# Performance work log

Measured on AMD Instinct MI355X. Metric: run time of the kernel, lower is better.

## Reference

```python
import jax, jax.numpy as jnp
import numpy as np

VOCAB = 32000
D_MODEL = 1024
PATCH_LEN = 16
NHEAD = 8
B = 8
S = 4096


def setup_inputs() -> dict:
    key = jax.random.key(0)
    ks = jax.random.split(key, 8)
    token_inputs = jax.random.randint(ks[0], (B, S), 0, VOCAB, dtype=jnp.int64 if jax.config.jax_enable_x64 else jnp.int32)
    attention_mask = jax.random.randint(ks[1], (B, S), 0, 2).astype(bool)
    emb_weight = jax.random.normal(ks[2], (VOCAB, D_MODEL), dtype=jnp.float32) * 0.02
    patch_query = jax.random.normal(ks[3], (1, 1, D_MODEL), dtype=jnp.float32) * 0.02
    # nn.MultiheadAttention packed in-projection [3D, D] and out projection [D, D]
    lim = 1.0 / np.sqrt(D_MODEL)
    in_proj_w = jax.random.uniform(ks[4], (3 * D_MODEL, D_MODEL), jnp.float32, -lim, lim)
    in_proj_b = jnp.zeros((3 * D_MODEL,), jnp.float32)
    out_w = jax.random.uniform(ks[5], (D_MODEL, D_MODEL), jnp.float32, -lim, lim)
    out_b = jnp.zeros((D_MODEL,), jnp.float32)
    return {
        "token_inputs": token_inputs,
        "attention_mask": attention_mask,
        "emb_weight": emb_weight,
        "patch_query": patch_query,
        "in_proj_w": in_proj_w,
        "in_proj_b": in_proj_b,
        "out_w": out_w,
        "out_b": out_b,
    }


def reference(token_inputs, attention_mask, emb_weight, patch_query, in_proj_w, in_proj_b, out_w, out_b):
    d_model = emb_weight.shape[1]
    h, dh = NHEAD, d_model // NHEAD
    L = PATCH_LEN

    tok_emb = emb_weight[token_inputs]              # [B, S, D]
    bsz, seqlen, _ = tok_emb.shape
    # seqlen chosen divisible by PATCH_LEN -> pad_len == 0 (matches torch path)
    num_patches = seqlen // L
    BP = bsz * num_patches
    patch_tokens = tok_emb.reshape(BP, L, d_model)  # [BP, L, D]
    patch_mask = attention_mask.reshape(BP, L)      # True = valid token

    patch_valid = patch_mask.any(axis=1)            # [BP]
    # force position 0 valid for fully-empty patches (safe softmax)
    safe_mask = patch_mask | ((~patch_valid)[:, None] & (jnp.arange(L) == 0)[None, :])

    wq, wk, wv = jnp.split(in_proj_w, 3, axis=0)    # each [D, D]
    bq, bk, bv = jnp.split(in_proj_b, 3, axis=0)

    q = patch_query[0, 0] @ wq.T + bq               # [D] (same query for all patches)
    k = patch_tokens @ wk.T + bk                    # [BP, L, D]
    v = patch_tokens @ wv.T + bv                    # [BP, L, D]

    qh = q.reshape(h, dh)                           # [H, dh]
    kh = k.reshape(BP, L, h, dh)                    # [BP, L, H, dh]
    vh = v.reshape(BP, L, h, dh)

    scale = 1.0 / jnp.sqrt(jnp.asarray(dh, q.dtype))
    scores = jnp.einsum('hd,blhd->bhl', qh, kh) * scale   # [BP, H, L]
    scores = jnp.where(safe_mask[:, None, :], scores, -jnp.inf)
    attn = jax.nn.softmax(scores, axis=-1)                # [BP, H, L]

    ctx = jnp.einsum('bhl,blhd->bhd', attn, vh).reshape(BP, d_model)
    patch_latent = ctx @ out_w.T + out_b                  # [BP, D]

    patch_latent = patch_latent.reshape(bsz, num_patches, d_model)
    pv = patch_valid.reshape(bsz, num_patches)
    patch_latent = patch_latent * pv[..., None].astype(patch_latent.dtype)
    return patch_latent, pv
```

## Files before the change

kernel.cpp:

```cpp
#include <hip/hip_runtime.h>
#include <stdint.h>

#define OUT_LATENT (2048*1024)
#define SCALE 0.08838834764831845f

typedef float f32x4v __attribute__((ext_vector_type(4)));
typedef short s16x8  __attribute__((ext_vector_type(8)));

static __device__ inline unsigned short f2bf(float f) {
    union { float f; uint32_t u; } v; v.f = f;
    uint32_t u = v.u;
    return (unsigned short)((u + 0x7FFFu + ((u >> 16) & 1u)) >> 16);
}
static __device__ inline float bflo(uint32_t u) {
    union { uint32_t u; float f; } v; v.u = u << 16; return v.f;
}
static __device__ inline float bfhi(uint32_t u) {
    union { uint32_t u; float f; } v; v.u = u & 0xFFFF0000u; return v.f;
}

static __device__ __forceinline__ void async16(const unsigned short* g, unsigned short* l) {
    __builtin_amdgcn_global_load_lds(
        (const __attribute__((address_space(1))) void*)g,
        (__attribute__((address_space(3))) void*)l, 16, 0, 0);
}

__global__ __launch_bounds__(256) void k_convw(
    const float* __restrict__ wv_src, const float* __restrict__ ow_src,
    unsigned short* __restrict__ wv_dst, unsigned short* __restrict__ ow_dst) {
    int t = threadIdx.x, b = blockIdx.x;
    const float* src; unsigned short* dst; int idx;
    if (b < 1024) { src = wv_src; dst = wv_dst; idx = b * 1024 + t * 4; }
    else          { src = ow_src; dst = ow_dst; idx = (b - 1024) * 1024 + t * 4; }
    float4 f = *(const float4*)(src + idx);
    ushort4 o; o.x = f2bf(f.x); o.y = f2bf(f.y); o.z = f2bf(f.z); o.w = f2bf(f.w);
    *(ushort4*)(dst + idx) = o;
}

__global__ __launch_bounds__(256) void k_qvec(
    const float* __restrict__ pq, const float* __restrict__ ipw,
    const float* __restrict__ ipb, float* __restrict__ qv) {
    int t = threadIdx.x, wave = t >> 6, lane = t & 63;
    int d = blockIdx.x * 4 + wave;
    const float* wrow = ipw + (size_t)d * 1024;
    float acc = 0.f;
    #pragma unroll
    for (int i = 0; i < 16; ++i) { int j = lane + i * 64; acc = fmaf(pq[j], wrow[j], acc); }
    #pragma unroll
    for (int m = 32; m >= 1; m >>= 1) acc += __shfl_xor(acc, m);
    if (lane == 0) qv[d] = acc + ipb[d];
}

__global__ __launch_bounds__(256) void k_qk(
    const float* __restrict__ qv, const float* __restrict__ ipw,
    const float* __restrict__ ipb, unsigned short* __restrict__ qkb,
    float* __restrict__ sb) {
    __shared__ float qs[128];
    __shared__ float part[128];
    int h = blockIdx.x, jseg = blockIdx.y, t = threadIdx.x;
    int jl = t & 127, dh = t >> 7;
    if (t < 128) qs[t] = qv[h * 128 + t];
    __syncthreads();
    float acc = 0.f;
    const float* wbase = ipw + (size_t)(1024 + h * 128 + dh * 64) * 1024 + jseg * 128 + jl;
    #pragma unroll 8
    for (int d = 0; d < 64; ++d)
        acc = fmaf(qs[dh * 64 + d], wbase[(size_t)d * 1024], acc);
    if (dh) part[jl] = acc;
    __syncthreads();
    if (!dh) qkb[h * 1024 + jseg * 128 + jl] = f2bf((acc + part[jl]) * SCALE);
    if (jseg == 0 && t < 64) {
        const float* bk = ipb + 1024 + h * 128;
        float p = qs[t] * bk[t] + qs[t + 64] * bk[t + 64];
        #pragma unroll
        for (int m = 32; m >= 1; m >>= 1) p += __shfl_xor(p, m);
        if (t == 0) sb[h] = p * SCALE;
    }
}

__global__ __launch_bounds__(256) void k_attn(
    const int* __restrict__ tok_ids, const int* __restrict__ amask,
    const float* __restrict__ emb, const unsigned short* __restrict__ qkb,
    const float* __restrict__ sb, unsigned short* __restrict__ Mout,
    float* __restrict__ pv) {
    __shared__ unsigned short tokL[16][1032];
    __shared__ float scoresP[4][16][8];
    __shared__ float attnL[16][8];
    __shared__ int allzL;

    int bp = blockIdx.x, t = threadIdx.x;
    int wave = t >> 6, lane = t & 63, lrow = lane & 15, quad = lane >> 4;

    s16x8 bfr[8];
    {
        const unsigned short* qbase = qkb + (lane & 7) * 1024 + wave * 256 + quad * 8;
        #pragma unroll
        for (int s = 0; s < 8; ++s) bfr[s] = *(const s16x8*)(qbase + s * 32);
    }

    {
        int row = t >> 4, c = t & 15;
        int tid = tok_ids[bp * 16 + row];
        const float* erow = emb + (size_t)tid * 1024;
        #pragma unroll
        for (int i = 0; i < 16; ++i) {
            int j4 = c + i * 16;
            float4 f = *(const float4*)(erow + j4 * 4);
            ushort4 o; o.x = f2bf(f.x); o.y = f2bf(f.y); o.z = f2bf(f.z); o.w = f2bf(f.w);
            *(ushort4*)(&tokL[row][j4 * 4]) = o;
        }
    }
    if (t < 16) {
        int any = (amask[bp * 16 + t] != 0);
        any |= __shfl_xor(any, 1); any |= __shfl_xor(any, 2);
        any |= __shfl_xor(any, 4); any |= __shfl_xor(any, 8);
        if (t == 0) { pv[bp] = any ? 1.f : 0.f; allzL = any ? 0 : 1; }
    }
    __syncthreads();

    {
        f32x4v acc = (f32x4v){0.f, 0.f, 0.f, 0.f};
        const unsigned short* arow = &tokL[lrow][wave * 256 + quad * 8];
        #pragma unroll
        for (int s = 0; s < 8; ++s) {
            s16x8 af = *(const s16x8*)(arow + s * 32);
            acc = __builtin_amdgcn_mfma_f32_16x16x32_bf16(af, bfr[s], acc, 0, 0, 0);
        }
        if (lrow < 8) {
            #pragma unroll
            for (int r = 0; r < 4; ++r) scoresP[wave][quad * 4 + r][lrow] = acc[r];
        }
    }
    __syncthreads();

    if (t < 128) {
        int hh = t >> 4, ll = t & 15;
        float s = scoresP[0][ll][hh] + scoresP[1][ll][hh]
                + scoresP[2][ll][hh] + scoresP[3][ll][hh] + sb[hh];
        bool valid = (amask[bp * 16 + ll] != 0) || (allzL && ll == 0);
        s = valid ? s : -1e30f;
        float mx = s;
        mx = fmaxf(mx, __shfl_xor(mx, 1)); mx = fmaxf(mx, __shfl_xor(mx, 2));
        mx = fmaxf(mx, __shfl_xor(mx, 4)); mx = fmaxf(mx, __shfl_xor(mx, 8));
        float e = __expf(s - mx);
        float sum = e;
        sum += __shfl_xor(sum, 1); sum += __shfl_xor(sum, 2);
        sum += __shfl_xor(sum, 4); sum += __shfl_xor(sum, 8);
        attnL[ll][hh] = e / sum;
    }
    __syncthreads();

    float macc[8][4];
    #pragma unroll
    for (int h = 0; h < 8; ++h)
        #pragma unroll
        for (int c = 0; c < 4; ++c) macc[h][c] = 0.f;
    #pragma unroll
    for (int ll = 0; ll < 16; ++ll) {
        uint2 tv = *(const uint2*)(&tokL[ll][t * 4]);
        float t0 = bflo(tv.x), t1 = bfhi(tv.x), t2 = bflo(tv.y), t3 = bfhi(tv.y);
        float4 a0 = *(const float4*)(&attnL[ll][0]);
        float4 a1 = *(const float4*)(&attnL[ll][4]);
        macc[0][0] = fmaf(a0.x, t0, macc[0][0]); macc[0][1] = fmaf(a0.x, t1, macc[0][1]);
        macc[0][2] = fmaf(a0.x, t2, macc[0][2]); macc[0][3] = fmaf(a0.x, t3, macc[0][3]);
        macc[1][0] = fmaf(a0.y, t0, macc[1][0]); macc[1][1] = fmaf(a0.y, t1, macc[1][1]);
        macc[1][2] = fmaf(a0.y, t2, macc[1][2]); macc[1][3] = fmaf(a0.y, t3, macc[1][3]);
        macc[2][0] = fmaf(a0.z, t0, macc[2][0]); macc[2][1] = fmaf(a0.z, t1, macc[2][1]);
        macc[2][2] = fmaf(a0.z, t2, macc[2][2]); macc[2][3] = fmaf(a0.z, t3, macc[2][3]);
        macc[3][0] = fmaf(a0.w, t0, macc[3][0]); macc[3][1] = fmaf(a0.w, t1, macc[3][1]);
        macc[3][2] = fmaf(a0.w, t2, macc[3][2]); macc[3][3] = fmaf(a0.w, t3, macc[3][3]);
        macc[4][0] = fmaf(a1.x, t0, macc[4][0]); macc[4][1] = fmaf(a1.x, t1, macc[4][1]);
        macc[4][2] = fmaf(a1.x, t2, macc[4][2]); macc[4][3] = fmaf(a1.x, t3, macc[4][3]);
        macc[5][0] = fmaf(a1.y, t0, macc[5][0]); macc[5][1] = fmaf(a1.y, t1, macc[5][1]);
        macc[5][2] = fmaf(a1.y, t2, macc[5][2]); macc[5][3] = fmaf(a1.y, t3, macc[5][3]);
        macc[6][0] = fmaf(a1.z, t0, macc[6][0]); macc[6][1] = fmaf(a1.z, t1, macc[6][1]);
        macc[6][2] = fmaf(a1.z, t2, macc[6][2]); macc[6][3] = fmaf(a1.z, t3, macc[6][3]);
        macc[7][0] = fmaf(a1.w, t0, macc[7][0]); macc[7][1] = fmaf(a1.w, t1, macc[7][1]);
        macc[7][2] = fmaf(a1.w, t2, macc[7][2]); macc[7][3] = fmaf(a1.w, t3, macc[7][3]);
    }
    #pragma unroll
    for (int h = 0; h < 8; ++h) {
        ushort4 o;
        o.x = f2bf(macc[h][0]); o.y = f2bf(macc[h][1]);
        o.z = f2bf(macc[h][2]); o.w = f2bf(macc[h][3]);
        *(ushort4*)(Mout + ((size_t)(h * 2048 + bp)) * 1024 + t * 4) = o;
    }
}

__device__ __forceinline__ void gemm128_mainloop(
    const unsigned short* __restrict__ A, const unsigned short* __restrict__ B,
    unsigned short* As, unsigned short* Bs, f32x4v acc[4][4]) {
    int t = threadIdx.x;
    int wave = t >> 6, lane = t & 63, lrow = lane & 15, quad = lane >> 4;
    int wm = wave & 1, wn = wave >> 1;
    int srow = t >> 2, sseg = (t & 3) * 8;
    #pragma unroll
    for (int mi = 0; mi < 4; ++mi)
        #pragma unroll
        for (int ni = 0; ni < 4; ++ni) acc[mi][ni] = (f32x4v){0.f, 0.f, 0.f, 0.f};
    for (int step = 0; step < 32; ++step) {
        int k0 = step * 32;
        __syncthreads();
        async16(A + (size_t)srow * 1024 + k0 + sseg,        As + t * 8);
        async16(A + (size_t)(srow + 64) * 1024 + k0 + sseg, As + (256 + t) * 8);
        async16(B + (size_t)srow * 1024 + k0 + sseg,        Bs + t * 8);
        async16(B + (size_t)(srow + 64) * 1024 + k0 + sseg, Bs + (256 + t) * 8);
        __syncthreads();
        s16x8 af[4], bf[4];
        #pragma unroll
        for (int i = 0; i < 4; ++i) {
            af[i] = *(const s16x8*)(As + (wm * 64 + i * 16 + lrow) * 32 + quad * 8);
            bf[i] = *(const s16x8*)(Bs + (wn * 64 + i * 16 + lrow) * 32 + quad * 8);
        }
        #pragma unroll
        for (int mi = 0; mi < 4; ++mi)
            #pragma unroll
            for (int ni = 0; ni < 4; ++ni)
                acc[mi][ni] = __builtin_amdgcn_mfma_f32_16x16x32_bf16(af[mi], bf[ni], acc[mi][ni], 0, 0, 0);
    }
}

__global__ __launch_bounds__(256) void k_gemm_ctx(
    const unsigned short* __restrict__ M, const unsigned short* __restrict__ wv,
    const float* __restrict__ ipb, unsigned short* __restrict__ ctx) {
    __shared__ unsigned short As[128 * 32], Bs[128 * 32];
    int mb = blockIdx.x, h = blockIdx.y;
    f32x4v acc[4][4];
    gemm128_mainloop(M + ((size_t)h * 2048 + mb * 128) * 1024,
                     wv + (size_t)h * 128 * 1024, As, Bs, acc);
    int t = threadIdx.x, wave = t >> 6, lane = t & 63, lrow = lane & 15, quad = lane >> 4;
    int wm = wave & 1, wn = wave >> 1;
    #pragma unroll
    for (int ni = 0; ni < 4; ++ni) {
        int n_g = h * 128 + wn * 64 + ni * 16 + lrow;
        float bias = ipb[2048 + n_g];
        #pragma unroll
        for (int mi = 0; mi < 4; ++mi) {
            #pragma unroll
            for (int r = 0; r < 4; ++r) {
                int m_g = mb * 128 + wm * 64 + mi * 16 + quad * 4 + r;
                ctx[(size_t)m_g * 1024 + n_g] = f2bf(acc[mi][ni][r] + bias);
            }
        }
    }
}

__global__ __launch_bounds__(256) void k_gemm_out(
    const unsigned short* __restrict__ ctx, const unsigned short* __restrict__ ow,
    const float* __restrict__ outb, const float* __restrict__ pv,
    float* __restrict__ out) {
    __shared__ unsigned short As[128 * 32], Bs[128 * 32];
    int mb = blockIdx.x, nb = blockIdx.y;
    f32x4v acc[4][4];
    gemm128_mainloop(ctx + (size_t)mb * 128 * 1024,
                     ow + (size_t)nb * 128 * 1024, As, Bs, acc);
    int t = threadIdx.x, wave = t >> 6, lane = t & 63, lrow = lane & 15, quad = lane >> 4;
    int wm = wave & 1, wn = wave >> 1;
    #pragma unroll
    for (int ni = 0; ni < 4; ++ni) {
        int n_g = nb * 128 + wn * 64 + ni * 16 + lrow;
        float bias = outb[n_g];
        #pragma unroll
        for (int mi = 0; mi < 4; ++mi) {
            #pragma unroll
            for (int r = 0; r < 4; ++r) {
                int m_g = mb * 128 + wm * 64 + mi * 16 + quad * 4 + r;
                out[(size_t)m_g * 1024 + n_g] = (acc[mi][ni][r] + bias) * pv[m_g];
            }
        }
    }
    if (nb == 0 && t < 128) out[OUT_LATENT + mb * 128 + t] = pv[mb * 128 + t];
}

extern "C" void kernel_launch(void* const* d_in, const int* in_sizes, int n_in,
                              void* d_out, int out_size, void* d_ws, size_t ws_size,
                              hipStream_t stream) {
    const int*   tok = (const int*)d_in[0];
    const int*   msk = (const int*)d_in[1];
    const float* emb = (const float*)d_in[2];
    const float* pq  = (const float*)d_in[3];
    const float* ipw = (const float*)d_in[4];
    const float* ipb = (const float*)d_in[5];
    const float* ow  = (const float*)d_in[6];
    const float* ob  = (const float*)d_in[7];
    float* out = (float*)d_out;
    char* ws = (char*)d_ws;

    float*          q_f   = (float*)(ws + 0);
    float*          sb_f  = (float*)(ws + 4096);
    float*          pv_f  = (float*)(ws + 8192);
    unsigned short* qk_b  = (unsigned short*)(ws + 16384);
    unsigned short* wv_b  = (unsigned short*)(ws + 32768);
    unsigned short* ow_b  = (unsigned short*)(ws + 32768 + 2097152);
    unsigned short* ctx_b = (unsigned short*)(ws + 32768 + 2 * 2097152);
    unsigned short* M_b   = (unsigned short*)(ws + 32768 + 2 * 2097152 + 4194304);

    k_convw<<<dim3(2048), dim3(256), 0, stream>>>(ipw + (size_t)2048 * 1024, ow, wv_b, ow_b);
    k_qvec <<<dim3(256),  dim3(256), 0, stream>>>(pq, ipw, ipb, q_f);
    k_qk   <<<dim3(8, 8), dim3(256), 0, stream>>>(q_f, ipw, ipb, qk_b, sb_f);
    k_attn <<<dim3(2048), dim3(256), 0, stream>>>(tok, msk, emb, qk_b, sb_f, M_b, pv_f);
    k_gemm_ctx<<<dim3(16, 8), dim3(256), 0, stream>>>(M_b, wv_b, ipb, ctx_b);
    k_gemm_out<<<dim3(16, 8), dim3(256), 0, stream>>>(ctx_b, ow_b, ob, pv_f, out);
}
```

Measured before the change: 267.3 us.

## Fuse prep kernels into one launch and double-buffer smaller GEMM tiles

Merges the weight bf16 conversion, q-vector projection and q·Wk folding into a single k_prep launch. Each qk block now recomputes its head's 128-element q slice itself, which removes two launches and a global round trip. The two bf16 GEMMs switch from 128x128 to 64x128 tiles, doubling the grid from 128 to 256 blocks to better fill the CUs. They also use a double-buffered LDS pipeline with one barrier per k-step, so the next tile's loads overlap the current MFMAs. The cost is redundant q computation across the eight jseg blocks per head and lower per-block reuse of the B tile.

```diff
diff --git a/kernel.cpp b/kernel.cpp
--- a/kernel.cpp
+++ b/kernel.cpp
@@ -25,42 +25,46 @@
         (__attribute__((address_space(3))) void*)l, 16, 0, 0);
 }
 
-__global__ __launch_bounds__(256) void k_convw(
-    const float* __restrict__ wv_src, const float* __restrict__ ow_src,
-    unsigned short* __restrict__ wv_dst, unsigned short* __restrict__ ow_dst) {
-    int t = threadIdx.x, b = blockIdx.x;
-    const float* src; unsigned short* dst; int idx;
-    if (b < 1024) { src = wv_src; dst = wv_dst; idx = b * 1024 + t * 4; }
-    else          { src = ow_src; dst = ow_dst; idx = (b - 1024) * 1024 + t * 4; }
-    float4 f = *(const float4*)(src + idx);
-    ushort4 o; o.x = f2bf(f.x); o.y = f2bf(f.y); o.z = f2bf(f.z); o.w = f2bf(f.w);
-    *(ushort4*)(dst + idx) = o;
-}
-
-__global__ __launch_bounds__(256) void k_qvec(
-    const float* __restrict__ pq, const float* __restrict__ ipw,
-    const float* __restrict__ ipb, float* __restrict__ qv) {
-    int t = threadIdx.x, wave = t >> 6, lane = t & 63;
-    int d = blockIdx.x * 4 + wave;
-    const float* wrow = ipw + (size_t)d * 1024;
-    float acc = 0.f;
-    #pragma unroll
-    for (int i = 0; i < 16; ++i) { int j = lane + i * 64; acc = fmaf(pq[j], wrow[j], acc); }
-    #pragma unroll
-    for (int m = 32; m >= 1; m >>= 1) acc += __shfl_xor(acc, m);
-    if (lane == 0) qv[d] = acc + ipb[d];
-}
-
-__global__ __launch_bounds__(256) void k_qk(
-    const float* __restrict__ qv, const float* __restrict__ ipw,
-    const float* __restrict__ ipb, unsigned short* __restrict__ qkb,
-    float* __restrict__ sb) {
+__global__ __launch_bounds__(256) void k_prep(
+    const float* __restrict__ ipw, const float* __restrict__ ipb,
+    const float* __restrict__ pq, const float* __restrict__ ow,
+    unsigned short* __restrict__ wv_dst, unsigned short* __restrict__ ow_dst,
+    unsigned short* __restrict__ qkb, float* __restrict__ sb) {
     __shared__ float qs[128];
     __shared__ float part[128];
-    int h = blockIdx.x, jseg = blockIdx.y, t = threadIdx.x;
+    int t = threadIdx.x, b = blockIdx.x;
+
+    if (b < 2048) {
+        const float* src; unsigned short* dst; int idx;
+        if (b < 1024) { src = ipw + (size_t)2048 * 1024; dst = wv_dst; idx = b * 1024 + t * 4; }
+        else          { src = ow;                        dst = ow_dst; idx = (b - 1024) * 1024 + t * 4; }
+        float4 f = *(const float4*)(src + idx);
+        ushort4 o; o.x = f2bf(f.x); o.y = f2bf(f.y); o.z = f2bf(f.z); o.w = f2bf(f.w);
+        *(ushort4*)(dst + idx) = o;
+        return;
+    }
+
+    int bb = b - 2048;
+    int h = bb >> 3, jseg = bb & 7;
+
+    {
+        int dl = t >> 1, half = t & 1;
+        const float* wrow = ipw + (size_t)(h * 128 + dl) * 1024 + half * 512;
+        const float* pqh = pq + half * 512;
+        float a = 0.f;
+        #pragma unroll 8
+        for (int j = 0; j < 512; j += 4) {
+            float4 w = *(const float4*)(wrow + j);
+            float4 p = *(const float4*)(pqh + j);
+            a = fmaf(w.x, p.x, a); a = fmaf(w.y, p.y, a);
+            a = fmaf(w.z, p.z, a); a = fmaf(w.w, p.w, a);
+        }
+        a += __shfl_xor(a, 1);
+        if (!half) qs[dl] = a + ipb[h * 128 + dl];
+    }
+    __syncthreads();
+
     int jl = t & 127, dh = t >> 7;
-    if (t < 128) qs[t] = qv[h * 128 + t];
-    __syncthreads();
     float acc = 0.f;
     const float* wbase = ipw + (size_t)(1024 + h * 128 + dh * 64) * 1024 + jseg * 128 + jl;
     #pragma unroll 8
@@ -187,35 +191,41 @@
     }
 }
 
-__device__ __forceinline__ void gemm128_mainloop(
+__device__ __forceinline__ void gemm64x128_dbuf(
     const unsigned short* __restrict__ A, const unsigned short* __restrict__ B,
-    unsigned short* As, unsigned short* Bs, f32x4v acc[4][4]) {
+    unsigned short* As, unsigned short* Bs, f32x4v acc[4][2]) {
     int t = threadIdx.x;
     int wave = t >> 6, lane = t & 63, lrow = lane & 15, quad = lane >> 4;
-    int wm = wave & 1, wn = wave >> 1;
-    int srow = t >> 2, sseg = (t & 3) * 8;
+    int r4 = t >> 2, seg = (t & 3) * 8;
     #pragma unroll
     for (int mi = 0; mi < 4; ++mi)
         #pragma unroll
-        for (int ni = 0; ni < 4; ++ni) acc[mi][ni] = (f32x4v){0.f, 0.f, 0.f, 0.f};
-    for (int step = 0; step < 32; ++step) {
-        int k0 = step * 32;
+        for (int ni = 0; ni < 2; ++ni) acc[mi][ni] = (f32x4v){0.f, 0.f, 0.f, 0.f};
+    async16(A + (size_t)r4 * 1024 + seg,        As + t * 8);
+    async16(B + (size_t)r4 * 1024 + seg,        Bs + t * 8);
+    async16(B + (size_t)(r4 + 64) * 1024 + seg, Bs + (256 + t) * 8);
+    for (int s = 0; s < 32; ++s) {
         __syncthreads();
-        async16(A + (size_t)srow * 1024 + k0 + sseg,        As + t * 8);
-        async16(A + (size_t)(srow + 64) * 1024 + k0 + sseg, As + (256 + t) * 8);
-        async16(B + (size_t)srow * 1024 + k0 + sseg,        Bs + t * 8);
-        async16(B + (size_t)(srow + 64) * 1024 + k0 + sseg, Bs + (256 + t) * 8);
-        __syncthreads();
-        s16x8 af[4], bf[4];
-        #pragma unroll
-        for (int i = 0; i < 4; ++i) {
-            af[i] = *(const s16x8*)(As + (wm * 64 + i * 16 + lrow) * 32 + quad * 8);
-            bf[i] = *(const s16x8*)(Bs + (wn * 64 + i * 16 + lrow) * 32 + quad * 8);
-        }
+        if (s < 31) {
+            int nk = (s + 1) * 32;
+            int pb = (s + 1) & 1;
+            async16(A + (size_t)r4 * 1024 + nk + seg,        As + pb * 2048 + t * 8);
+            async16(B + (size_t)r4 * 1024 + nk + seg,        Bs + pb * 4096 + t * 8);
+            async16(B + (size_t)(r4 + 64) * 1024 + nk + seg, Bs + pb * 4096 + (256 + t) * 8);
+        }
+        const unsigned short* Asc = As + (s & 1) * 2048;
+        const unsigned short* Bsc = Bs + (s & 1) * 4096;
+        s16x8 af[4], bf[2];
+        #pragma unroll
+        for (int mi = 0; mi < 4; ++mi)
+            af[mi] = *(const s16x8*)(Asc + (mi * 16 + lrow) * 32 + quad * 8);
+        #pragma unroll
+        for (int ni = 0; ni < 2; ++ni)
+            bf[ni] = *(const s16x8*)(Bsc + (wave * 32 + ni * 16 + lrow) * 32 + quad * 8);
         #pragma unroll
         for (int mi = 0; mi < 4; ++mi)
             #pragma unroll
-            for (int ni = 0; ni < 4; ++ni)
+            for (int ni = 0; ni < 2; ++ni)
                 acc[mi][ni] = __builtin_amdgcn_mfma_f32_16x16x32_bf16(af[mi], bf[ni], acc[mi][ni], 0, 0, 0);
     }
 }
@@ -223,22 +233,21 @@
 __global__ __launch_bounds__(256) void k_gemm_ctx(
     const unsigned short* __restrict__ M, const unsigned short* __restrict__ wv,
     const float* __restrict__ ipb, unsigned short* __restrict__ ctx) {
-    __shared__ unsigned short As[128 * 32], Bs[128 * 32];
+    __shared__ unsigned short As[2 * 2048], Bs[2 * 4096];
     int mb = blockIdx.x, h = blockIdx.y;
-    f32x4v acc[4][4];
-    gemm128_mainloop(M + ((size_t)h * 2048 + mb * 128) * 1024,
-                     wv + (size_t)h * 128 * 1024, As, Bs, acc);
+    f32x4v acc[4][2];
+    gemm64x128_dbuf(M + ((size_t)h * 2048 + mb * 64) * 1024,
+                    wv + (size_t)h * 128 * 1024, As, Bs, acc);
     int t = threadIdx.x, wave = t >> 6, lane = t & 63, lrow = lane & 15, quad = lane >> 4;
-    int wm = wave & 1, wn = wave >> 1;
-    #pragma unroll
-    for (int ni = 0; ni < 4; ++ni) {
-        int n_g = h * 128 + wn * 64 + ni * 16 + lrow;
+    #pragma unroll
+    for (int ni = 0; ni < 2; ++ni) {
+        int n_g = h * 128 + wave * 32 + ni * 16 + lrow;
         float bias = ipb[2048 + n_g];
         #pragma unroll
         for (int mi = 0; mi < 4; ++mi) {
             #pragma unroll
             for (int r = 0; r < 4; ++r) {
-                int m_g = mb * 128 + wm * 64 + mi * 16 + quad * 4 + r;
+                int m_g = mb * 64 + mi * 16 + quad * 4 + r;
                 ctx[(size_t)m_g * 1024 + n_g] = f2bf(acc[mi][ni][r] + bias);
             }
         }
@@ -249,27 +258,26 @@
     const unsigned short* __restrict__ ctx, const unsigned short* __restrict__ ow,
     const float* __restrict__ outb, const float* __restrict__ pv,
     float* __restrict__ out) {
-    __shared__ unsigned short As[128 * 32], Bs[128 * 32];
+    __shared__ unsigned short As[2 * 2048], Bs[2 * 4096];
     int mb = blockIdx.x, nb = blockIdx.y;
-    f32x4v acc[4][4];
-    gemm128_mainloop(ctx + (size_t)mb * 128 * 1024,
-                     ow + (size_t)nb * 128 * 1024, As, Bs, acc);
+    f32x4v acc[4][2];
+    gemm64x128_dbuf(ctx + (size_t)mb * 64 * 1024,
+                    ow + (size_t)nb * 128 * 1024, As, Bs, acc);
     int t = threadIdx.x, wave = t >> 6, lane = t & 63, lrow = lane & 15, quad = lane >> 4;
-    int wm = wave & 1, wn = wave >> 1;
-    #pragma unroll
-    for (int ni = 0; ni < 4; ++ni) {
-        int n_g = nb * 128 + wn * 64 + ni * 16 + lrow;
+    #pragma unroll
+    for (int ni = 0; ni < 2; ++ni) {
+        int n_g = nb * 128 + wave * 32 + ni * 16 + lrow;
         float bias = outb[n_g];
         #pragma unroll
         for (int mi = 0; mi < 4; ++mi) {
             #pragma unroll
             for (int r = 0; r < 4; ++r) {
-                int m_g = mb * 128 + wm * 64 + mi * 16 + quad * 4 + r;
+                int m_g = mb * 64 + mi * 16 + quad * 4 + r;
                 out[(size_t)m_g * 1024 + n_g] = (acc[mi][ni][r] + bias) * pv[m_g];
             }
         }
     }
-    if (nb == 0 && t < 128) out[OUT_LATENT + mb * 128 + t] = pv[mb * 128 + t];
+    if (nb == 0 && t < 64) out[OUT_LATENT + mb * 64 + t] = pv[mb * 64 + t];
 }
 
 extern "C" void kernel_launch(void* const* d_in, const int* in_sizes, int n_in,
@@ -286,7 +294,6 @@
     float* out = (float*)d_out;
     char* ws = (char*)d_ws;
 
-    float*          q_f   = (float*)(ws + 0);
     float*          sb_f  = (float*)(ws + 4096);
     float*          pv_f  = (float*)(ws + 8192);
     unsigned short* qk_b  = (unsigned short*)(ws + 16384);
@@ -295,10 +302,8 @@
     unsigned short* ctx_b = (unsigned short*)(ws + 32768 + 2 * 2097152);
     unsigned short* M_b   = (unsigned short*)(ws + 32768 + 2 * 2097152 + 4194304);
 
-    k_convw<<<dim3(2048), dim3(256), 0, stream>>>(ipw + (size_t)2048 * 1024, ow, wv_b, ow_b);
-    k_qvec <<<dim3(256),  dim3(256), 0, stream>>>(pq, ipw, ipb, q_f);
-    k_qk   <<<dim3(8, 8), dim3(256), 0, stream>>>(q_f, ipw, ipb, qk_b, sb_f);
-    k_attn <<<dim3(2048), dim3(256), 0, stream>>>(tok, msk, emb, qk_b, sb_f, M_b, pv_f);
-    k_gemm_ctx<<<dim3(16, 8), dim3(256), 0, stream>>>(M_b, wv_b, ipb, ctx_b);
-    k_gemm_out<<<dim3(16, 8), dim3(256), 0, stream>>>(ctx_b, ow_b, ob, pv_f, out);
-}
+    k_prep<<<dim3(2112), dim3(256), 0, stream>>>(ipw, ipb, pq, ow, wv_b, ow_b, qk_b, sb_f);
+    k_attn<<<dim3(2048), dim3(256), 0, stream>>>(tok, msk, emb, qk_b, sb_f, M_b, pv_f);
+    k_gemm_ctx<<<dim3(32, 8), dim3(256), 0, stream>>>(M_b, wv_b, ipb, ctx_b);
+    k_gemm_out<<<dim3(32, 8), dim3(256), 0, stream>>>(ctx_b, ow_b, ob, pv_f, out);
+}
```

Result: slower. 300.6 us (+12.5%).
